# Optimization experiments

Measured on AMD Instinct MI355X. Metric: run time of the kernel, lower is better.

Reference implementation:

```python
import jax, jax.numpy as jnp
import numpy as np

BUCKET_SIZE = 64  # init kwarg bucket_size
DIM = 64          # init kwarg dim (per-head dim, used for scaling)


def setup_inputs() -> dict:
    key = jax.random.key(0)
    kq, kk = jax.random.split(key)
    q = jax.random.normal(kq, (32, 8192, 64), dtype=jnp.float32)
    k = jax.random.normal(kk, (32, 8192, 64), dtype=jnp.float32)
    return {"q": q, "k": k}


def _cumavg(t):
    # cumulative average along the sequence axis (axis=1)
    r = jnp.arange(1, t.shape[1] + 1, dtype=t.dtype)
    return jnp.cumsum(t, axis=1) / r[None, :, None]


def reference(q, k):
    bh, n, d = q.shape
    buckets = n // BUCKET_SIZE
    kv_buckets = k.shape[1] // BUCKET_SIZE

    # bucket the cumulative averages: [bh, buckets, bucket_size, d]
    q_r = _cumavg(q).reshape(bh, buckets, BUCKET_SIZE, d)
    k_r = _cumavg(k).reshape(bh, kv_buckets, BUCKET_SIZE, d)

    sq = q_r[:, :, 0]                                   # [bh, buckets, d]
    sk = k_r.sum(axis=2)                                # [bh, kv_buckets, d]
    sk = jnp.pad(sk, ((0, 0), (1, 0), (0, 0)))          # pad one zero bucket row at front

    R = jnp.einsum('bie,bje->bij', sq, sk) * (DIM ** -0.5)  # [bh, buckets, kv_buckets+1]

    rows = jnp.arange(buckets)[:, None]
    cols = jnp.arange(kv_buckets + 1)[None, :]
    neg = -jnp.finfo(R.dtype).max
    # masked_fill: for row i, columns i+1..buckets set to -max (cols > rows)
    R = jnp.where(cols > rows, neg, R)
    R = jax.nn.softmax(R, axis=-1)
    # tril(diagonal=-1): keep entries with col < row
    R = jnp.where(cols < rows, R, jnp.zeros((), R.dtype))
    return R
```

## Files before the change

kernel.cpp:

```cpp
#include <hip/hip_runtime.h>
#include <cstddef>

constexpr int BH = 32;
constexpr int N  = 8192;
constexpr int D  = 64;
constexpr int BK = 64;
constexpr int NB = 128;
constexpr int NC = 129;

__global__ __launch_bounds__(256) void kA(const float* __restrict__ q,
                                          const float* __restrict__ k,
                                          float* __restrict__ qsum,
                                          float* __restrict__ ksum,
                                          float* __restrict__ kw,
                                          float* __restrict__ qfirst,
                                          float* __restrict__ W) {
  const int tid  = threadIdx.x;
  const int wv   = tid >> 6;
  const int lane = tid & 63;
  const int f    = lane & 15;
  const int r0   = lane >> 4;
  const int j    = blockIdx.x * 4 + wv;
  const int b    = blockIdx.y;
  const int base = j * BK;

  const float4* q4 = (const float4*)(q + ((size_t)b * N + base) * D);
  const float4* k4 = (const float4*)(k + ((size_t)b * N + base) * D);

  float aq[4] = {0,0,0,0}, ak[4] = {0,0,0,0}, aw[4] = {0,0,0,0};
  float qf[4] = {0,0,0,0};
  float wh = 0.0f;

#pragma unroll
  for (int t = 15; t >= 0; --t) {
    const int row = (r0 << 4) + t;
    wh += 1.0f / (float)(base + row + 1);
    const float4 qv = q4[row * 16 + f];
    const float4 kv = k4[row * 16 + f];
    aq[0] += qv.x; aq[1] += qv.y; aq[2] += qv.z; aq[3] += qv.w;
    ak[0] += kv.x; ak[1] += kv.y; ak[2] += kv.z; ak[3] += kv.w;
    aw[0] += kv.x * wh; aw[1] += kv.y * wh; aw[2] += kv.z * wh; aw[3] += kv.w * wh;
    if (t == 0 && r0 == 0) { qf[0] = qv.x; qf[1] = qv.y; qf[2] = qv.z; qf[3] = qv.w; }
  }

  const float w16 = __shfl_xor(wh, 16);
  const float w32 = __shfl_xor(wh, 32);
  const float w48 = __shfl_xor(wh, 48);
  float TU = 0.0f;
  if ((r0 ^ 1) > r0) TU += w16;
  if ((r0 ^ 2) > r0) TU += w32;
  if ((r0 ^ 3) > r0) TU += w48;
  const float Wfull = wh + w16 + w32 + w48;

#pragma unroll
  for (int c = 0; c < 4; ++c) aw[c] += TU * ak[c];

#pragma unroll
  for (int c = 0; c < 4; ++c) {
    aq[c] += __shfl_xor(aq[c], 16); aq[c] += __shfl_xor(aq[c], 32);
    ak[c] += __shfl_xor(ak[c], 16); ak[c] += __shfl_xor(ak[c], 32);
    aw[c] += __shfl_xor(aw[c], 16); aw[c] += __shfl_xor(aw[c], 32);
  }

  if (r0 == 0) {
    const size_t ob = ((size_t)b * NB + j) * D;
    ((float4*)(qsum   + ob))[f] = make_float4(aq[0], aq[1], aq[2], aq[3]);
    ((float4*)(ksum   + ob))[f] = make_float4(ak[0], ak[1], ak[2], ak[3]);
    ((float4*)(kw     + ob))[f] = make_float4(aw[0], aw[1], aw[2], aw[3]);
    ((float4*)(qfirst + ob))[f] = make_float4(qf[0], qf[1], qf[2], qf[3]);
    if (f == 0 && b == 0) W[j] = Wfull;
  }
}

__global__ __launch_bounds__(256) void kB(const float* __restrict__ qsum,
                                          const float* __restrict__ ksum,
                                          const float* __restrict__ kw,
                                          const float* __restrict__ qfirst,
                                          const float* __restrict__ W,
                                          float* __restrict__ sq,
                                          float* __restrict__ skp) {
  const int side = blockIdx.x;
  const int b    = blockIdx.y;
  const int tid  = threadIdx.x;
  const int d    = tid & 63;
  const int jg   = tid >> 6;

  __shared__ float buf[NB * D];
  __shared__ float tot[4 * D];
  __shared__ float Wl[NB];

  const float* src = (side == 0 ? qsum : ksum) + (size_t)b * NB * D;
  {
    const float4* g4 = (const float4*)src;
    float4* l4 = (float4*)buf;
    for (int u = tid; u < NB * D / 4; u += 256) l4[u] = g4[u];
    if (side == 1 && tid < NB) Wl[tid] = W[tid];
  }
  __syncthreads();

  float t0 = 0.0f;
  for (int jj = 0; jj < 32; ++jj) t0 += buf[(jg * 32 + jj) * D + d];
  tot[jg * D + d] = t0;
  __syncthreads();

  float pre = 0.0f;
  for (int g = 0; g < jg; ++g) pre += tot[g * D + d];

  if (side == 0) {
    for (int jj = 0; jj < 32; ++jj) {
      const int j = jg * 32 + jj;
      const size_t o = ((size_t)b * NB + j) * D + d;
      sq[o] = (pre + qfirst[o]) / (float)(j * BK + 1);
      pre += buf[j * D + d];
    }
  } else {
    if (tid < D) skp[(size_t)b * NC * D + tid] = 0.0f;
    for (int jj = 0; jj < 32; ++jj) {
      const int j = jg * 32 + jj;
      const size_t o = ((size_t)b * NB + j) * D + d;
      skp[((size_t)b * NC + j + 1) * D + d] = pre * Wl[j] + kw[o];
      pre += buf[j * D + d];
    }
  }
}

__global__ __launch_bounds__(128) void kC(const float* __restrict__ sq,
                                          const float* __restrict__ skp,
                                          float* __restrict__ out) {
  const int i   = blockIdx.x;
  const int b   = blockIdx.y;
  const int tid = threadIdx.x;
  const int wv  = tid >> 6;

  __shared__ float srow[D];
  __shared__ float wred[2][2];

  if (tid < 16)
    ((float4*)srow)[tid] = ((const float4*)(sq + ((size_t)b * NB + i) * D))[tid];
  __syncthreads();

  const int j = tid;
  const bool valid = (j <= i);
  float dot = 0.0f;
  if (valid) {
    const float4* kr = (const float4*)(skp + ((size_t)b * NC + j) * D);
    const float4* sr = (const float4*)srow;
#pragma unroll
    for (int f = 0; f < 16; ++f) {
      const float4 a = sr[f];
      const float4 c = kr[f];
      dot += a.x * c.x + a.y * c.y + a.z * c.z + a.w * c.w;
    }
    dot *= 0.125f;
  }

  float m = valid ? dot : -3.402823466e38f;
#pragma unroll
  for (int s = 32; s; s >>= 1) m = fmaxf(m, __shfl_xor(m, s));
  if ((tid & 63) == 0) wred[0][wv] = m;
  __syncthreads();
  const float mx = fmaxf(wred[0][0], wred[0][1]);

  const float e = valid ? expf(dot - mx) : 0.0f;
  float ss = e;
#pragma unroll
  for (int s = 32; s; s >>= 1) ss += __shfl_xor(ss, s);
  if ((tid & 63) == 0) wred[1][wv] = ss;
  __syncthreads();
  const float denom = wred[1][0] + wred[1][1];

  float* orow = out + ((size_t)b * NB + i) * NC;
  orow[j] = (j < i) ? (e / denom) : 0.0f;
  if (tid == 0) orow[128] = 0.0f;
}

extern "C" void kernel_launch(void* const* d_in, const int* in_sizes, int n_in,
                              void* d_out, int out_size, void* d_ws, size_t ws_size,
                              hipStream_t stream) {
  const float* q = (const float*)d_in[0];
  const float* k = (const float*)d_in[1];
  float* out = (float*)d_out;

  float* ws     = (float*)d_ws;
  float* qsum   = ws;
  float* ksum   = qsum   + (size_t)BH * NB * D;
  float* kw     = ksum   + (size_t)BH * NB * D;
  float* qfirst = kw     + (size_t)BH * NB * D;
  float* sq     = qfirst + (size_t)BH * NB * D;
  float* skp    = sq     + (size_t)BH * NB * D;
  float* W      = skp    + (size_t)BH * NC * D;

  kA<<<dim3(NB / 4, BH), 256, 0, stream>>>(q, k, qsum, ksum, kw, qfirst, W);
  kB<<<dim3(2, BH), 256, 0, stream>>>(qsum, ksum, kw, qfirst, W, sq, skp);
  kC<<<dim3(NB, BH), 128, 0, stream>>>(sq, skp, out);
}
```

Baseline: 176.2 us.

## Fuse prefix-scan and softmax kernels, split bucket reduction across q/k blocks

The bucket reduction kernel now runs one block per bucket and per side (q or k), and computes the tail weights with a wave-level scan. It also reduces across waves through shared memory. The scan and softmax kernels are merged into one kernel that keeps the scanned k summaries in a rotated, bank-conflict-avoiding shared layout and computes 16 query rows per block. This removes a launch and the global round trip of sq/skp. Each of the 8 tiles per head redundantly recomputes the k prefix scan, and there are fewer blocks for the final stage.

```diff
diff --git a/kernel.cpp b/kernel.cpp
--- a/kernel.cpp
+++ b/kernel.cpp
@@ -15,163 +15,197 @@
                                           float* __restrict__ kw,
                                           float* __restrict__ qfirst,
                                           float* __restrict__ W) {
-  const int tid  = threadIdx.x;
-  const int wv   = tid >> 6;
-  const int lane = tid & 63;
-  const int f    = lane & 15;
-  const int r0   = lane >> 4;
-  const int j    = blockIdx.x * 4 + wv;
-  const int b    = blockIdx.y;
+  const int j = blockIdx.x, b = blockIdx.y, side = blockIdx.z;
+  const int tid = threadIdx.x;
+  const int f = tid & 15, r = tid >> 4, w = tid >> 6, lane = tid & 63;
   const int base = j * BK;
 
-  const float4* q4 = (const float4*)(q + ((size_t)b * N + base) * D);
-  const float4* k4 = (const float4*)(k + ((size_t)b * N + base) * D);
-
-  float aq[4] = {0,0,0,0}, ak[4] = {0,0,0,0}, aw[4] = {0,0,0,0};
-  float qf[4] = {0,0,0,0};
-  float wh = 0.0f;
-
-#pragma unroll
-  for (int t = 15; t >= 0; --t) {
-    const int row = (r0 << 4) + t;
-    wh += 1.0f / (float)(base + row + 1);
-    const float4 qv = q4[row * 16 + f];
-    const float4 kv = k4[row * 16 + f];
-    aq[0] += qv.x; aq[1] += qv.y; aq[2] += qv.z; aq[3] += qv.w;
-    ak[0] += kv.x; ak[1] += kv.y; ak[2] += kv.z; ak[3] += kv.w;
-    aw[0] += kv.x * wh; aw[1] += kv.y * wh; aw[2] += kv.z * wh; aw[3] += kv.w * wh;
-    if (t == 0 && r0 == 0) { qf[0] = qv.x; qf[1] = qv.y; qf[2] = qv.z; qf[3] = qv.w; }
-  }
-
-  const float w16 = __shfl_xor(wh, 16);
-  const float w32 = __shfl_xor(wh, 32);
-  const float w48 = __shfl_xor(wh, 48);
-  float TU = 0.0f;
-  if ((r0 ^ 1) > r0) TU += w16;
-  if ((r0 ^ 2) > r0) TU += w32;
-  if ((r0 ^ 3) > r0) TU += w48;
-  const float Wfull = wh + w16 + w32 + w48;
-
-#pragma unroll
-  for (int c = 0; c < 4; ++c) aw[c] += TU * ak[c];
+  __shared__ float tailw[BK];
+  __shared__ float red[2][4][D];
+
+  const float* src = (side == 0 ? q : k) + ((size_t)b * N + base) * D;
+  const float4* s4 = (const float4*)src;
+
+  float4 v[4];
+#pragma unroll
+  for (int p = 0; p < 4; ++p) v[p] = s4[(r + 16 * p) * 16 + f];
+
+  if (side == 1) {
+    if (w == 0) {
+      float x = 1.0f / (float)(base + lane + 1);
+#pragma unroll
+      for (int s = 1; s < 64; s <<= 1) {
+        float y = __shfl_down(x, s, 64);
+        if (lane + s < 64) x += y;
+      }
+      tailw[lane] = x;
+      if (lane == 0 && b == 0) W[j] = x;
+    }
+    __syncthreads();
+  }
+
+  float a0[4] = {0, 0, 0, 0}, a1[4] = {0, 0, 0, 0};
+  if (side == 0) {
+#pragma unroll
+    for (int p = 0; p < 4; ++p) {
+      a0[0] += v[p].x; a0[1] += v[p].y; a0[2] += v[p].z; a0[3] += v[p].w;
+    }
+  } else {
+#pragma unroll
+    for (int p = 0; p < 4; ++p) {
+      const float tw = tailw[r + 16 * p];
+      a0[0] += v[p].x; a0[1] += v[p].y; a0[2] += v[p].z; a0[3] += v[p].w;
+      a1[0] += v[p].x * tw; a1[1] += v[p].y * tw;
+      a1[2] += v[p].z * tw; a1[3] += v[p].w * tw;
+    }
+  }
 
 #pragma unroll
   for (int c = 0; c < 4; ++c) {
-    aq[c] += __shfl_xor(aq[c], 16); aq[c] += __shfl_xor(aq[c], 32);
-    ak[c] += __shfl_xor(ak[c], 16); ak[c] += __shfl_xor(ak[c], 32);
-    aw[c] += __shfl_xor(aw[c], 16); aw[c] += __shfl_xor(aw[c], 32);
-  }
-
-  if (r0 == 0) {
-    const size_t ob = ((size_t)b * NB + j) * D;
-    ((float4*)(qsum   + ob))[f] = make_float4(aq[0], aq[1], aq[2], aq[3]);
-    ((float4*)(ksum   + ob))[f] = make_float4(ak[0], ak[1], ak[2], ak[3]);
-    ((float4*)(kw     + ob))[f] = make_float4(aw[0], aw[1], aw[2], aw[3]);
-    ((float4*)(qfirst + ob))[f] = make_float4(qf[0], qf[1], qf[2], qf[3]);
-    if (f == 0 && b == 0) W[j] = Wfull;
+    a0[c] += __shfl_xor(a0[c], 16, 64); a0[c] += __shfl_xor(a0[c], 32, 64);
+    a1[c] += __shfl_xor(a1[c], 16, 64); a1[c] += __shfl_xor(a1[c], 32, 64);
+  }
+  if (lane < 16) {
+    ((float4*)&red[0][w][0])[f] = make_float4(a0[0], a0[1], a0[2], a0[3]);
+    ((float4*)&red[1][w][0])[f] = make_float4(a1[0], a1[1], a1[2], a1[3]);
+  }
+  __syncthreads();
+
+  const size_t ob = ((size_t)b * NB + j) * D;
+  if (tid < D) {
+    const float s0 = red[0][0][tid] + red[0][1][tid] + red[0][2][tid] + red[0][3][tid];
+    if (side == 0) {
+      qsum[ob + tid] = s0;
+    } else {
+      ksum[ob + tid] = s0;
+      kw[ob + tid] = red[1][0][tid] + red[1][1][tid] + red[1][2][tid] + red[1][3][tid];
+    }
+  }
+  if (side == 0 && r == 0) {
+    ((float4*)(qfirst + ob))[f] = v[0];
   }
 }
 
-__global__ __launch_bounds__(256) void kB(const float* __restrict__ qsum,
-                                          const float* __restrict__ ksum,
-                                          const float* __restrict__ kw,
-                                          const float* __restrict__ qfirst,
-                                          const float* __restrict__ W,
-                                          float* __restrict__ sq,
-                                          float* __restrict__ skp) {
-  const int side = blockIdx.x;
-  const int b    = blockIdx.y;
-  const int tid  = threadIdx.x;
-  const int d    = tid & 63;
-  const int jg   = tid >> 6;
+__global__ __launch_bounds__(256) void kBC(const float* __restrict__ qsum,
+                                           const float* __restrict__ ksum,
+                                           const float* __restrict__ kw,
+                                           const float* __restrict__ qfirst,
+                                           const float* __restrict__ W,
+                                           float* __restrict__ out) {
+  const int tile = blockIdx.x, b = blockIdx.y;
+  const int tid = threadIdx.x;
+  const int d = tid & 63, g = tid >> 6;
+  const int jp = tid & 63, rep = tid >> 6;
 
   __shared__ float buf[NB * D];
-  __shared__ float tot[4 * D];
+  __shared__ float skpS[NB * D];
+  __shared__ float sqs[16 * D];
+  __shared__ float tots[4 * D];
   __shared__ float Wl[NB];
 
-  const float* src = (side == 0 ? qsum : ksum) + (size_t)b * NB * D;
-  {
-    const float4* g4 = (const float4*)src;
+  const size_t bb = (size_t)b * NB * D;
+
+  {
+    const float4* g4 = (const float4*)(qsum + bb);
     float4* l4 = (float4*)buf;
     for (int u = tid; u < NB * D / 4; u += 256) l4[u] = g4[u];
-    if (side == 1 && tid < NB) Wl[tid] = W[tid];
-  }
-  __syncthreads();
-
-  float t0 = 0.0f;
-  for (int jj = 0; jj < 32; ++jj) t0 += buf[(jg * 32 + jj) * D + d];
-  tot[jg * D + d] = t0;
-  __syncthreads();
-
-  float pre = 0.0f;
-  for (int g = 0; g < jg; ++g) pre += tot[g * D + d];
-
-  if (side == 0) {
+
+    const float4* qf4 = (const float4*)(qfirst + bb + (size_t)tile * 16 * D);
+    float4* sq4 = (float4*)sqs;
+    sq4[tid] = qf4[tid];
+
+    if (tid < NB) Wl[tid] = W[tid];
+
+    const float4* kw4 = (const float4*)(kw + bb);
+    for (int u = tid; u < 127 * 16; u += 256) {
+      const int row = (u >> 4) + 1, f = u & 15;
+      ((float4*)skpS)[row * 16 + ((f + row) & 15)] = kw4[u];
+    }
+    if (tid < D) skpS[tid] = 0.0f;
+  }
+  __syncthreads();
+
+  const int T0 = tile * 16;
+  {
+    const int span = T0 >> 2;
+    float t0 = 0.0f;
+    for (int jj = g * span; jj < (g + 1) * span; ++jj) t0 += buf[jj * D + d];
+    tots[g * D + d] = t0;
+  }
+  __syncthreads();
+  if (tid < D) {
+    float pre = tots[d] + tots[D + d] + tots[2 * D + d] + tots[3 * D + d];
+    for (int ii = 0; ii < 16; ++ii) {
+      const int i = T0 + ii;
+      sqs[ii * D + d] = (pre + sqs[ii * D + d]) / (float)(i * BK + 1);
+      pre += buf[i * D + d];
+    }
+  }
+  __syncthreads();
+
+  {
+    const float4* g4 = (const float4*)(ksum + bb);
+    float4* l4 = (float4*)buf;
+    for (int u = tid; u < NB * D / 4; u += 256) l4[u] = g4[u];
+  }
+  __syncthreads();
+  {
+    float t0 = 0.0f;
+    for (int jj = g * 32; jj < (g + 1) * 32; ++jj) t0 += buf[jj * D + d];
+    tots[g * D + d] = t0;
+  }
+  __syncthreads();
+  {
+    float pre = 0.0f;
+    for (int gg = 0; gg < g; ++gg) pre += tots[gg * D + d];
     for (int jj = 0; jj < 32; ++jj) {
-      const int j = jg * 32 + jj;
-      const size_t o = ((size_t)b * NB + j) * D + d;
-      sq[o] = (pre + qfirst[o]) / (float)(j * BK + 1);
+      const int j = g * 32 + jj;
+      if (j < 127) {
+        const int row = j + 1;
+        const int idx = row * D + (((d >> 2) + row) & 15) * 4 + (d & 3);
+        skpS[idx] = pre * Wl[j] + skpS[idx];
+      }
       pre += buf[j * D + d];
     }
-  } else {
-    if (tid < D) skp[(size_t)b * NC * D + tid] = 0.0f;
-    for (int jj = 0; jj < 32; ++jj) {
-      const int j = jg * 32 + jj;
-      const size_t o = ((size_t)b * NB + j) * D + d;
-      skp[((size_t)b * NC + j + 1) * D + d] = pre * Wl[j] + kw[o];
-      pre += buf[j * D + d];
-    }
-  }
-}
-
-__global__ __launch_bounds__(128) void kC(const float* __restrict__ sq,
-                                          const float* __restrict__ skp,
-                                          float* __restrict__ out) {
-  const int i   = blockIdx.x;
-  const int b   = blockIdx.y;
-  const int tid = threadIdx.x;
-  const int wv  = tid >> 6;
-
-  __shared__ float srow[D];
-  __shared__ float wred[2][2];
-
-  if (tid < 16)
-    ((float4*)srow)[tid] = ((const float4*)(sq + ((size_t)b * NB + i) * D))[tid];
-  __syncthreads();
-
-  const int j = tid;
-  const bool valid = (j <= i);
-  float dot = 0.0f;
-  if (valid) {
-    const float4* kr = (const float4*)(skp + ((size_t)b * NC + j) * D);
-    const float4* sr = (const float4*)srow;
-#pragma unroll
-    for (int f = 0; f < 16; ++f) {
-      const float4 a = sr[f];
-      const float4 c = kr[f];
-      dot += a.x * c.x + a.y * c.y + a.z * c.z + a.w * c.w;
-    }
-    dot *= 0.125f;
-  }
-
-  float m = valid ? dot : -3.402823466e38f;
-#pragma unroll
-  for (int s = 32; s; s >>= 1) m = fmaxf(m, __shfl_xor(m, s));
-  if ((tid & 63) == 0) wred[0][wv] = m;
-  __syncthreads();
-  const float mx = fmaxf(wred[0][0], wred[0][1]);
-
-  const float e = valid ? expf(dot - mx) : 0.0f;
-  float ss = e;
-#pragma unroll
-  for (int s = 32; s; s >>= 1) ss += __shfl_xor(ss, s);
-  if ((tid & 63) == 0) wred[1][wv] = ss;
-  __syncthreads();
-  const float denom = wred[1][0] + wred[1][1];
-
-  float* orow = out + ((size_t)b * NB + i) * NC;
-  orow[j] = (j < i) ? (e / denom) : 0.0f;
-  if (tid == 0) orow[128] = 0.0f;
+  }
+  __syncthreads();
+
+  float acc0[4] = {0, 0, 0, 0}, acc1[4] = {0, 0, 0, 0};
+  const float4* sk4 = (const float4*)skpS;
+  const float4* sq4 = (const float4*)sqs;
+#pragma unroll
+  for (int d4 = 0; d4 < 16; ++d4) {
+    const int slot = (d4 + jp) & 15;
+    const float4 k0 = sk4[jp * 16 + slot];
+    const float4 k1 = sk4[(jp + 64) * 16 + slot];
+#pragma unroll
+    for (int ii = 0; ii < 4; ++ii) {
+      const float4 s = sq4[(rep * 4 + ii) * 16 + d4];
+      acc0[ii] += s.x * k0.x + s.y * k0.y + s.z * k0.z + s.w * k0.w;
+      acc1[ii] += s.x * k1.x + s.y * k1.y + s.z * k1.z + s.w * k1.w;
+    }
+  }
+
+#pragma unroll
+  for (int ii = 0; ii < 4; ++ii) {
+    const int i = T0 + rep * 4 + ii;
+    const int j0 = jp, j1 = jp + 64;
+    const float v0 = acc0[ii] * 0.125f, v1 = acc1[ii] * 0.125f;
+    const bool val0 = (j0 <= i), val1 = (j1 <= i);
+    float m = fmaxf(val0 ? v0 : -3.402823466e38f, val1 ? v1 : -3.402823466e38f);
+#pragma unroll
+    for (int s = 1; s < 64; s <<= 1) m = fmaxf(m, __shfl_xor(m, s, 64));
+    const float e0 = val0 ? __expf(v0 - m) : 0.0f;
+    const float e1 = val1 ? __expf(v1 - m) : 0.0f;
+    float ss = e0 + e1;
+#pragma unroll
+    for (int s = 1; s < 64; s <<= 1) ss += __shfl_xor(ss, s, 64);
+    const float rden = 1.0f / ss;
+    float* orow = out + ((size_t)b * NB + i) * NC;
+    orow[j0] = (j0 < i) ? e0 * rden : 0.0f;
+    orow[j1] = (j1 < i) ? e1 * rden : 0.0f;
+    if (jp == 0) orow[128] = 0.0f;
+  }
 }
 
 extern "C" void kernel_launch(void* const* d_in, const int* in_sizes, int n_in,
@@ -186,11 +220,8 @@
   float* ksum   = qsum   + (size_t)BH * NB * D;
   float* kw     = ksum   + (size_t)BH * NB * D;
   float* qfirst = kw     + (size_t)BH * NB * D;
-  float* sq     = qfirst + (size_t)BH * NB * D;
-  float* skp    = sq     + (size_t)BH * NB * D;
-  float* W      = skp    + (size_t)BH * NC * D;
-
-  kA<<<dim3(NB / 4, BH), 256, 0, stream>>>(q, k, qsum, ksum, kw, qfirst, W);
-  kB<<<dim3(2, BH), 256, 0, stream>>>(qsum, ksum, kw, qfirst, W, sq, skp);
-  kC<<<dim3(NB, BH), 128, 0, stream>>>(sq, skp, out);
+  float* W      = qfirst + (size_t)BH * NB * D;
+
+  kA<<<dim3(NB, BH, 2), 256, 0, stream>>>(q, k, qsum, ksum, kw, qfirst, W);
+  kBC<<<dim3(8, BH), 256, 0, stream>>>(qsum, ksum, kw, qfirst, W, out);
 }
```

Result: faster. 158.8 us (-9.8%).

## Split q/k reduction across grid z and tile softmax rows with shared skp

Applied to the files above, without the earlier changes.

kA now processes q and k in separate blocks along a new grid z dimension, loading all 16 rows per lane up front to expose more memory-level parallelism. kC now handles 8 query rows per block, staging the needed skp rows into a rotation-swizzled shared buffer and reusing them across rows, with wave-level softmax reductions and fast exp. This reduces redundant global reads of skp and block count, at the cost of larger LDS use and more registers per thread.

```diff
diff --git a/kernel.cpp b/kernel.cpp
--- a/kernel.cpp
+++ b/kernel.cpp
@@ -15,60 +15,75 @@
                                           float* __restrict__ kw,
                                           float* __restrict__ qfirst,
                                           float* __restrict__ W) {
-  const int tid  = threadIdx.x;
-  const int wv   = tid >> 6;
-  const int lane = tid & 63;
+  const int wv   = threadIdx.x >> 6;
+  const int lane = threadIdx.x & 63;
   const int f    = lane & 15;
-  const int r0   = lane >> 4;
+  const int r    = lane >> 4;
   const int j    = blockIdx.x * 4 + wv;
   const int b    = blockIdx.y;
+  const int side = blockIdx.z;
   const int base = j * BK;
-
-  const float4* q4 = (const float4*)(q + ((size_t)b * N + base) * D);
-  const float4* k4 = (const float4*)(k + ((size_t)b * N + base) * D);
-
-  float aq[4] = {0,0,0,0}, ak[4] = {0,0,0,0}, aw[4] = {0,0,0,0};
-  float qf[4] = {0,0,0,0};
-  float wh = 0.0f;
-
-#pragma unroll
-  for (int t = 15; t >= 0; --t) {
-    const int row = (r0 << 4) + t;
-    wh += 1.0f / (float)(base + row + 1);
-    const float4 qv = q4[row * 16 + f];
-    const float4 kv = k4[row * 16 + f];
-    aq[0] += qv.x; aq[1] += qv.y; aq[2] += qv.z; aq[3] += qv.w;
-    ak[0] += kv.x; ak[1] += kv.y; ak[2] += kv.z; ak[3] += kv.w;
-    aw[0] += kv.x * wh; aw[1] += kv.y * wh; aw[2] += kv.z * wh; aw[3] += kv.w * wh;
-    if (t == 0 && r0 == 0) { qf[0] = qv.x; qf[1] = qv.y; qf[2] = qv.z; qf[3] = qv.w; }
-  }
-
-  const float w16 = __shfl_xor(wh, 16);
-  const float w32 = __shfl_xor(wh, 32);
-  const float w48 = __shfl_xor(wh, 48);
-  float TU = 0.0f;
-  if ((r0 ^ 1) > r0) TU += w16;
-  if ((r0 ^ 2) > r0) TU += w32;
-  if ((r0 ^ 3) > r0) TU += w48;
-  const float Wfull = wh + w16 + w32 + w48;
-
-#pragma unroll
-  for (int c = 0; c < 4; ++c) aw[c] += TU * ak[c];
-
-#pragma unroll
-  for (int c = 0; c < 4; ++c) {
-    aq[c] += __shfl_xor(aq[c], 16); aq[c] += __shfl_xor(aq[c], 32);
-    ak[c] += __shfl_xor(ak[c], 16); ak[c] += __shfl_xor(ak[c], 32);
-    aw[c] += __shfl_xor(aw[c], 16); aw[c] += __shfl_xor(aw[c], 32);
-  }
-
-  if (r0 == 0) {
-    const size_t ob = ((size_t)b * NB + j) * D;
-    ((float4*)(qsum   + ob))[f] = make_float4(aq[0], aq[1], aq[2], aq[3]);
-    ((float4*)(ksum   + ob))[f] = make_float4(ak[0], ak[1], ak[2], ak[3]);
-    ((float4*)(kw     + ob))[f] = make_float4(aw[0], aw[1], aw[2], aw[3]);
-    ((float4*)(qfirst + ob))[f] = make_float4(qf[0], qf[1], qf[2], qf[3]);
-    if (f == 0 && b == 0) W[j] = Wfull;
+  const size_t ob = ((size_t)b * NB + j) * D;
+
+  const float* src = (side == 0 ? q : k) + ((size_t)b * N + base) * D;
+  const float4* s4 = (const float4*)src;
+
+  if (side == 0) {
+    float4 v[16];
+#pragma unroll
+    for (int p = 0; p < 16; ++p) v[p] = s4[(r * 16 + p) * 16 + f];
+
+    float a[4] = {0, 0, 0, 0};
+#pragma unroll
+    for (int p = 0; p < 16; ++p) {
+      a[0] += v[p].x; a[1] += v[p].y; a[2] += v[p].z; a[3] += v[p].w;
+    }
+#pragma unroll
+    for (int c = 0; c < 4; ++c) {
+      a[c] += __shfl_xor(a[c], 16, 64);
+      a[c] += __shfl_xor(a[c], 32, 64);
+    }
+    if (r == 0) {
+      ((float4*)(qsum + ob))[f] = make_float4(a[0], a[1], a[2], a[3]);
+      ((float4*)(qfirst + ob))[f] = v[0];
+    }
+  } else {
+    float4 v[16];
+#pragma unroll
+    for (int p = 0; p < 16; ++p) v[p] = s4[(r * 16 + 15 - p) * 16 + f];
+
+    float ak[4] = {0, 0, 0, 0}, aw[4] = {0, 0, 0, 0};
+    float wh = 0.0f;
+#pragma unroll
+    for (int p = 0; p < 16; ++p) {
+      const int row = r * 16 + 15 - p;
+      wh += 1.0f / (float)(base + row + 1);
+      ak[0] += v[p].x; ak[1] += v[p].y; ak[2] += v[p].z; ak[3] += v[p].w;
+      aw[0] += v[p].x * wh; aw[1] += v[p].y * wh;
+      aw[2] += v[p].z * wh; aw[3] += v[p].w * wh;
+    }
+
+    const float w16 = __shfl_xor(wh, 16, 64);
+    const float w32 = __shfl_xor(wh, 32, 64);
+    const float w48 = __shfl_xor(wh, 48, 64);
+    float TU = 0.0f;
+    if ((r ^ 1) > r) TU += w16;
+    if ((r ^ 2) > r) TU += w32;
+    if ((r ^ 3) > r) TU += w48;
+    const float Wfull = wh + w16 + w32 + w48;
+
+#pragma unroll
+    for (int c = 0; c < 4; ++c) aw[c] += TU * ak[c];
+#pragma unroll
+    for (int c = 0; c < 4; ++c) {
+      ak[c] += __shfl_xor(ak[c], 16, 64); ak[c] += __shfl_xor(ak[c], 32, 64);
+      aw[c] += __shfl_xor(aw[c], 16, 64); aw[c] += __shfl_xor(aw[c], 32, 64);
+    }
+    if (r == 0) {
+      ((float4*)(ksum + ob))[f] = make_float4(ak[0], ak[1], ak[2], ak[3]);
+      ((float4*)(kw   + ob))[f] = make_float4(aw[0], aw[1], aw[2], aw[3]);
+      if (lane == 0 && b == 0) W[j] = Wfull;
+    }
   }
 }
 
@@ -124,54 +139,65 @@
   }
 }
 
-__global__ __launch_bounds__(128) void kC(const float* __restrict__ sq,
+__global__ __launch_bounds__(256) void kC(const float* __restrict__ sq,
                                           const float* __restrict__ skp,
                                           float* __restrict__ out) {
-  const int i   = blockIdx.x;
-  const int b   = blockIdx.y;
+  const int tile = blockIdx.x, b = blockIdx.y;
   const int tid = threadIdx.x;
-  const int wv  = tid >> 6;
-
-  __shared__ float srow[D];
-  __shared__ float wred[2][2];
-
-  if (tid < 16)
-    ((float4*)srow)[tid] = ((const float4*)(sq + ((size_t)b * NB + i) * D))[tid];
+  const int jp = tid & 63, rep = tid >> 6;
+  const int T0 = tile * 8;
+  const int rows = T0 + 8;
+
+  __shared__ float skpS[NB * D];
+  __shared__ float sqs[8 * D];
+
+  {
+    const float4* g4 = (const float4*)(skp + (size_t)b * NC * D);
+    for (int u = tid; u < rows * 16; u += 256) {
+      const int row = u >> 4, f = u & 15;
+      ((float4*)skpS)[row * 16 + ((f + row) & 15)] = g4[u];
+    }
+    if (tid < 128)
+      ((float4*)sqs)[tid] = ((const float4*)(sq + ((size_t)b * NB + T0) * D))[tid];
+  }
   __syncthreads();
 
-  const int j = tid;
-  const bool valid = (j <= i);
-  float dot = 0.0f;
-  if (valid) {
-    const float4* kr = (const float4*)(skp + ((size_t)b * NC + j) * D);
-    const float4* sr = (const float4*)srow;
-#pragma unroll
-    for (int f = 0; f < 16; ++f) {
-      const float4 a = sr[f];
-      const float4 c = kr[f];
-      dot += a.x * c.x + a.y * c.y + a.z * c.z + a.w * c.w;
-    }
-    dot *= 0.125f;
-  }
-
-  float m = valid ? dot : -3.402823466e38f;
-#pragma unroll
-  for (int s = 32; s; s >>= 1) m = fmaxf(m, __shfl_xor(m, s));
-  if ((tid & 63) == 0) wred[0][wv] = m;
-  __syncthreads();
-  const float mx = fmaxf(wred[0][0], wred[0][1]);
-
-  const float e = valid ? expf(dot - mx) : 0.0f;
-  float ss = e;
-#pragma unroll
-  for (int s = 32; s; s >>= 1) ss += __shfl_xor(ss, s);
-  if ((tid & 63) == 0) wred[1][wv] = ss;
-  __syncthreads();
-  const float denom = wred[1][0] + wred[1][1];
-
-  float* orow = out + ((size_t)b * NB + i) * NC;
-  orow[j] = (j < i) ? (e / denom) : 0.0f;
-  if (tid == 0) orow[128] = 0.0f;
+  float acc0[2] = {0, 0}, acc1[2] = {0, 0};
+  const float4* sk4 = (const float4*)skpS;
+  const float4* sq4 = (const float4*)sqs;
+#pragma unroll
+  for (int d4 = 0; d4 < 16; ++d4) {
+    const int slot = (d4 + jp) & 15;
+    const float4 k0 = sk4[jp * 16 + slot];
+    const float4 k1 = sk4[(jp + 64) * 16 + slot];
+#pragma unroll
+    for (int ii = 0; ii < 2; ++ii) {
+      const float4 s = sq4[(rep * 2 + ii) * 16 + d4];
+      acc0[ii] += s.x * k0.x + s.y * k0.y + s.z * k0.z + s.w * k0.w;
+      acc1[ii] += s.x * k1.x + s.y * k1.y + s.z * k1.z + s.w * k1.w;
+    }
+  }
+
+#pragma unroll
+  for (int ii = 0; ii < 2; ++ii) {
+    const int i = T0 + rep * 2 + ii;
+    const int j0 = jp, j1 = jp + 64;
+    const float v0 = acc0[ii] * 0.125f, v1 = acc1[ii] * 0.125f;
+    const bool val0 = (j0 <= i), val1 = (j1 <= i);
+    float m = fmaxf(val0 ? v0 : -3.402823466e38f, val1 ? v1 : -3.402823466e38f);
+#pragma unroll
+    for (int s = 1; s < 64; s <<= 1) m = fmaxf(m, __shfl_xor(m, s, 64));
+    const float e0 = val0 ? __expf(v0 - m) : 0.0f;
+    const float e1 = val1 ? __expf(v1 - m) : 0.0f;
+    float ss = e0 + e1;
+#pragma unroll
+    for (int s = 1; s < 64; s <<= 1) ss += __shfl_xor(ss, s, 64);
+    const float rden = 1.0f / ss;
+    float* orow = out + ((size_t)b * NB + i) * NC;
+    orow[j0] = (j0 < i) ? e0 * rden : 0.0f;
+    orow[j1] = (j1 < i) ? e1 * rden : 0.0f;
+    if (jp == 0) orow[128] = 0.0f;
+  }
 }
 
 extern "C" void kernel_launch(void* const* d_in, const int* in_sizes, int n_in,
@@ -190,7 +216,7 @@
   float* skp    = sq     + (size_t)BH * NB * D;
   float* W      = skp    + (size_t)BH * NC * D;
 
-  kA<<<dim3(NB / 4, BH), 256, 0, stream>>>(q, k, qsum, ksum, kw, qfirst, W);
+  kA<<<dim3(NB / 4, BH, 2), 256, 0, stream>>>(q, k, qsum, ksum, kw, qfirst, W);
   kB<<<dim3(2, BH), 256, 0, stream>>>(qsum, ksum, kw, qfirst, W, sq, skp);
-  kC<<<dim3(NB, BH), 128, 0, stream>>>(sq, skp, out);
-}
+  kC<<<dim3(16, BH), 256, 0, stream>>>(sq, skp, out);
+}
```

New measurement: 160.6 us. 1.1x faster.
